# Kernel optimization log

Measured on AMD Instinct MI355X. Metric: run time of the kernel, lower is better.

## Reference

```python
import jax, jax.numpy as jnp
import numpy as np

B, N, D_IN, D_OUT, H = 8, 1024, 768, 768, 12
D_HEAD = D_OUT // H  # 64; per-head softmax scale is sqrt(D_HEAD)


def setup_inputs() -> dict:
    key = jax.random.key(0)
    kx, kq, kk, kv, kwo, kbo = jax.random.split(key, 6)
    s_in = 1.0 / np.sqrt(D_IN)
    s_out = 1.0 / np.sqrt(D_OUT)
    return {
        "x": jax.random.normal(kx, (B, N, D_IN), dtype=jnp.float32),
        # stacked per-head Linear weights, torch layout [out, in] -> [H, d_head, D_IN]
        "Wq": jax.random.uniform(kq, (H, D_HEAD, D_IN), jnp.float32, -s_in, s_in),
        "Wk": jax.random.uniform(kk, (H, D_HEAD, D_IN), jnp.float32, -s_in, s_in),
        "Wv": jax.random.uniform(kv, (H, D_HEAD, D_IN), jnp.float32, -s_in, s_in),
        "Wo": jax.random.uniform(kwo, (D_OUT, D_OUT), jnp.float32, -s_out, s_out),
        "bo": jax.random.uniform(kbo, (D_OUT,), jnp.float32, -s_out, s_out),
    }


def reference(x, Wq, Wk, Wv, Wo, bo):
    # Per-head projections, batched over heads: [B, H, N, d_head]
    q = jnp.einsum('bnd,hed->bhne', x, Wq)
    k = jnp.einsum('bnd,hed->bhne', x, Wk)
    v = jnp.einsum('bnd,hed->bhne', x, Wv)
    scale = 1.0 / np.sqrt(D_HEAD)
    scores = jnp.einsum('bhie,bhje->bhij', q, k) * scale  # [B, H, N, N]
    att = jax.nn.softmax(scores, axis=-1)
    out = jnp.einsum('bhij,bhje->bhie', att, v)  # [B, H, N, d_head]
    # concat heads along last dim: [B, N, H*d_head]
    out = out.transpose(0, 2, 1, 3).reshape(B, N, D_OUT)
    return out @ Wo.T + bo
```

## Files before the change

### kernel.cpp

```cpp
#include <hip/hip_runtime.h>
#include <hip/hip_bf16.h>


typedef unsigned short u16;
typedef unsigned int u32;
typedef __attribute__((ext_vector_type(8))) short bf8;
typedef __attribute__((ext_vector_type(4))) short bf4;
typedef __attribute__((ext_vector_type(4))) float f4;
typedef __attribute__((ext_vector_type(4))) unsigned short us4;

#define NB 8
#define NSEQ 1024
#define DMODEL 768
#define NHEAD 12
#define DHEAD 64

#define XELEMS   (NB * NSEQ * DMODEL)
#define WELEMS   (DMODEL * DMODEL)

__device__ __forceinline__ float b2f(u16 u) {
  union { unsigned int i; float f; } c; c.i = ((unsigned int)u) << 16; return c.f;
}
__device__ __forceinline__ u16 f2b(float f) {
  union { float f; unsigned int i; } c; c.f = f;
  unsigned int r = c.i + 0x7fffu + ((c.i >> 16) & 1u);
  return (u16)(r >> 16);
}
__device__ __forceinline__ void gl_lds16(const u16* g, u16* l) {
  __builtin_amdgcn_global_load_lds(
      (const __attribute__((address_space(1))) unsigned int*)g,
      (__attribute__((address_space(3))) unsigned int*)l, 16, 0, 0);
}

struct CvtArgs {
  const float* src[5];
  u16* dst[5];
};
#define G0 (XELEMS / 4)
#define GW (WELEMS / 4)
#define GTOT (G0 + 4 * GW)

__global__ __launch_bounds__(256) void cvt_kernel(CvtArgs a) {
  size_t g = (size_t)blockIdx.x * 256 + threadIdx.x;
  if (g >= GTOT) return;
  int t; size_t off;
  if (g < G0) { t = 0; off = g; }
  else { size_t r = g - G0; t = 1 + (int)(r / GW); off = r % GW; }
  f4 v = *(const f4*)(a.src[t] + off * 4);
  us4 o;
  o[0] = f2b(v[0]); o[1] = f2b(v[1]); o[2] = f2b(v[2]); o[3] = f2b(v[3]);
  *(us4*)(a.dst[t] + off * 4) = o;
}

__global__ __launch_bounds__(256, 2) void qkv_gemm(
    const u16* __restrict__ x, const u16* __restrict__ Wq,
    const u16* __restrict__ Wk, const u16* __restrict__ Wv,
    u16* __restrict__ q, u16* __restrict__ k, u16* __restrict__ vt)
{
  __shared__ __align__(16) u16 lA[2][128 * 64];
  __shared__ __align__(16) u16 lB[2][128 * 64];

  const int tid  = threadIdx.x;
  const int lane = tid & 63;
  const int w    = tid >> 6;
  const int wm   = w >> 1;
  const int wn   = w & 1;
  const int col  = lane & 15;
  const int quad = lane >> 4;

  const int bid = blockIdx.x;
  const int xcd = bid & 7;
  const int j   = bid >> 3;
  const int bng = j / 48;
  const int rr  = j % 48;
  const int bm8 = rr / 6;
  const int bn6 = rr % 6;
  const int bm  = xcd * 8 + bm8;
  const int bn  = bng * 6 + bn6;

  const int m0 = bm * 128;
  const int proj = bn / 6;
  const u16* Wsel = (proj == 0) ? Wq : (proj == 1 ? Wk : Wv);
  const int nrem0 = (bn % 6) * 128;

  const int srow8 = lane >> 3;
  const int sg    = (lane & 7) ^ srow8;

  const u16* gA = x    + (size_t)(m0    + w * 32 + srow8) * DMODEL + sg * 8;
  const u16* gB = Wsel + (size_t)(nrem0 + w * 32 + srow8) * DMODEL + sg * 8;

  f4 acc[4][4];
#pragma unroll
  for (int i = 0; i < 4; i++)
#pragma unroll
    for (int jj = 0; jj < 4; jj++) acc[i][jj] = (f4)0.0f;

#define QKV_STAGE(T, BUF)                                                      \
  do {                                                                         \
    const int kk_ = (T) * 64;                                                  \
    _Pragma("unroll")                                                          \
    for (int i_ = 0; i_ < 4; i_++)                                             \
      gl_lds16(gA + (size_t)(i_ * 8) * DMODEL + kk_,                           \
               &lA[BUF][(w * 32 + i_ * 8) * 64]);                              \
    _Pragma("unroll")                                                          \
    for (int i_ = 0; i_ < 4; i_++)                                             \
      gl_lds16(gB + (size_t)(i_ * 8) * DMODEL + kk_,                           \
               &lB[BUF][(w * 32 + i_ * 8) * 64]);                              \
  } while (0)

  QKV_STAGE(0, 0);
  __syncthreads();

  for (int t = 0; t < 12; t++) {
    const int cur = t & 1;
    if (t < 11) QKV_STAGE(t + 1, cur ^ 1);

    bf8 af[4][2], bfr[4][2];
#pragma unroll
    for (int mt = 0; mt < 4; mt++) {
      const int row = wm * 64 + mt * 16 + col;
#pragma unroll
      for (int kt = 0; kt < 2; kt++)
        af[mt][kt] = *(const bf8*)&lA[cur][row * 64 + (((kt * 4 + quad) ^ (row & 7)) << 3)];
    }
#pragma unroll
    for (int nt = 0; nt < 4; nt++) {
      const int row = wn * 64 + nt * 16 + col;
#pragma unroll
      for (int kt = 0; kt < 2; kt++)
        bfr[nt][kt] = *(const bf8*)&lB[cur][row * 64 + (((kt * 4 + quad) ^ (row & 7)) << 3)];
    }

    __builtin_amdgcn_s_setprio(1);
#pragma unroll
    for (int mt = 0; mt < 4; mt++)
#pragma unroll
      for (int nt = 0; nt < 4; nt++)
#pragma unroll
        for (int kt = 0; kt < 2; kt++)
          acc[mt][nt] = __builtin_amdgcn_mfma_f32_16x16x32_bf16(af[mt][kt], bfr[nt][kt], acc[mt][nt], 0, 0, 0);
    __builtin_amdgcn_s_setprio(0);

    __syncthreads();
  }
#undef QKV_STAGE

  const int mw0 = m0 + wm * 64, nw0 = nrem0 + wn * 64;
  if (proj == 2) {
#pragma unroll
    for (int mt = 0; mt < 4; mt++) {
#pragma unroll
      for (int nt = 0; nt < 4; nt++) {
        const int nc = nw0 + nt * 16 + col;
        const int h = nc >> 6, e = nc & 63;
        const int t0 = mw0 + mt * 16 + quad * 4;
        const int b = t0 >> 10, tok0 = t0 & 1023;
        us4 pk;
#pragma unroll
        for (int r = 0; r < 4; r++) pk[r] = f2b(acc[mt][nt][r]);
        *(us4*)(vt + ((size_t)(b * NHEAD + h) * DHEAD + e) * NSEQ + tok0) = pk;
      }
    }
  } else {
    u16* dst = (proj == 0) ? q : k;
    const float scl = (proj == 0) ? 0.125f : 1.0f;
#pragma unroll
    for (int mt = 0; mt < 4; mt++) {
#pragma unroll
      for (int nt = 0; nt < 4; nt++) {
        const int nc = nw0 + nt * 16 + col;
        const int h = nc >> 6, e = nc & 63;
#pragma unroll
        for (int r = 0; r < 4; r++) {
          const int t = mw0 + mt * 16 + quad * 4 + r;
          const int b = t >> 10, tok = t & 1023;
          dst[((size_t)(b * NHEAD + h) * NSEQ + tok) * DHEAD + e] = f2b(acc[mt][nt][r] * scl);
        }
      }
    }
  }
}

__global__ __launch_bounds__(256, 3) void attn_kernel(
    const u16* __restrict__ q, const u16* __restrict__ k,
    const u16* __restrict__ vt, u16* __restrict__ attn)
{
  __shared__ __align__(16) u16 ldsK[2][64 * 64];
  __shared__ __align__(16) u16 ldsV[2][64 * 64];
  __shared__ __align__(16) u16 ldsP[4][32][72];

  const int tid  = threadIdx.x;
  const int lane = tid & 63;
  const int w    = tid >> 6;
  const int col  = lane & 15;
  const int quad = lane >> 4;

  const int idx = blockIdx.x;
  const int bh = idx % 96, qc = idx / 96;
  const int b = bh / 12, h = bh % 12;

  const size_t head = ((size_t)b * NHEAD + h) * NSEQ * DHEAD;
  const int q0 = qc * 128 + w * 32;

  const int srow8 = lane >> 3;
  const int sg    = (lane & 7) ^ srow8;

  bf8 onesf;
#pragma unroll
  for (int jj = 0; jj < 8; jj++) onesf[jj] = (short)0x3F80;

  bf8 qf[2][2];
#pragma unroll
  for (int qt = 0; qt < 2; qt++)
#pragma unroll
    for (int kt = 0; kt < 2; kt++) {
      const int row = q0 + qt * 16 + col;
      qf[qt][kt] = *(const bf8*)(q + head + (size_t)row * DHEAD + kt * 32 + quad * 8);
    }

  f4 lacc[2];
  f4 o[2][4];
#pragma unroll
  for (int mt = 0; mt < 2; mt++) {
    lacc[mt] = (f4)0.0f;
#pragma unroll
    for (int et = 0; et < 4; et++) o[mt][et] = (f4)0.0f;
  }

#pragma unroll
  for (int i = 0; i < 2; i++) {
    const int li = w * 2 + i;
    gl_lds16(k  + head + (size_t)(li * 8 + srow8) * DHEAD + sg * 8, &ldsK[0][li * 512]);
    gl_lds16(vt + head + (size_t)(li * 8 + srow8) * NSEQ + sg * 8,  &ldsV[0][li * 512]);
  }

  for (int t = 0; t < NSEQ / 64; t++) {
    const int cur = t & 1;
    __syncthreads();
    if (t < NSEQ / 64 - 1) {
      const int kb2 = (t + 1) * 64;
#pragma unroll
      for (int i = 0; i < 2; i++) {
        const int li = w * 2 + i;
        gl_lds16(k  + head + (size_t)(kb2 + li * 8 + srow8) * DHEAD + sg * 8,
                 &ldsK[cur ^ 1][li * 512]);
        gl_lds16(vt + head + (size_t)(li * 8 + srow8) * NSEQ + kb2 + sg * 8,
                 &ldsV[cur ^ 1][li * 512]);
      }
    }

    f4 st[4][2];
#pragma unroll
    for (int kvt = 0; kvt < 4; kvt++)
#pragma unroll
      for (int qt = 0; qt < 2; qt++) st[kvt][qt] = (f4)0.0f;
#pragma unroll
    for (int kt = 0; kt < 2; kt++) {
      bf8 kf[4];
#pragma unroll
      for (int kvt = 0; kvt < 4; kvt++) {
        const int row = kvt * 16 + col;
        kf[kvt] = *(const bf8*)&ldsK[cur][row * 64 + (((kt * 4 + quad) ^ (col & 7)) << 3)];
      }
      __builtin_amdgcn_s_setprio(1);
#pragma unroll
      for (int kvt = 0; kvt < 4; kvt++)
#pragma unroll
        for (int qt = 0; qt < 2; qt++)
          st[kvt][qt] = __builtin_amdgcn_mfma_f32_16x16x32_bf16(kf[kvt], qf[qt][kt], st[kvt][qt], 0, 0, 0);
      __builtin_amdgcn_s_setprio(0);
    }

#pragma unroll
    for (int kvt = 0; kvt < 4; kvt++)
#pragma unroll
      for (int qt = 0; qt < 2; qt++) {
        const f4 p = st[kvt][qt];
        bf4 pw;
        pw[0] = (short)f2b(__expf(p[0]));
        pw[1] = (short)f2b(__expf(p[1]));
        pw[2] = (short)f2b(__expf(p[2]));
        pw[3] = (short)f2b(__expf(p[3]));
        *(bf4*)&ldsP[w][qt * 16 + col][kvt * 16 + quad * 4] = pw;
      }
    asm volatile("" ::: "memory");

#pragma unroll
    for (int kt2 = 0; kt2 < 2; kt2++) {
      bf8 vf[4];
#pragma unroll
      for (int et = 0; et < 4; et++) {
        const int row = et * 16 + col;
        vf[et] = *(const bf8*)&ldsV[cur][row * 64 + (((kt2 * 4 + quad) ^ (col & 7)) << 3)];
      }
#pragma unroll
      for (int mt = 0; mt < 2; mt++) {
        const bf8 pf = *(const bf8*)&ldsP[w][mt * 16 + col][kt2 * 32 + quad * 8];
        __builtin_amdgcn_s_setprio(1);
        lacc[mt] = __builtin_amdgcn_mfma_f32_16x16x32_bf16(pf, onesf, lacc[mt], 0, 0, 0);
#pragma unroll
        for (int et = 0; et < 4; et++)
          o[mt][et] = __builtin_amdgcn_mfma_f32_16x16x32_bf16(pf, vf[et], o[mt][et], 0, 0, 0);
        __builtin_amdgcn_s_setprio(0);
      }
    }
  }

#pragma unroll
  for (int mt = 0; mt < 2; mt++)
#pragma unroll
    for (int r = 0; r < 4; r++) {
      const float inv = 1.0f / lacc[mt][r];
      const int token = q0 + mt * 16 + quad * 4 + r;
#pragma unroll
      for (int et = 0; et < 4; et++)
        attn[(size_t)(b * NSEQ + token) * DMODEL + h * DHEAD + et * 16 + col] =
            f2b(o[mt][et][r] * inv);
    }
}

__global__ __launch_bounds__(256, 2) void out_gemm(
    const u16* __restrict__ attn, const u16* __restrict__ Wo,
    const float* __restrict__ bo, float* __restrict__ out)
{
  __shared__ __align__(16) u16 lA[2][128 * 64];
  __shared__ __align__(16) u16 lB[2][128 * 64];

  const int tid  = threadIdx.x;
  const int lane = tid & 63;
  const int w    = tid >> 6;
  const int wm   = w >> 1;
  const int wn   = w & 1;
  const int col  = lane & 15;
  const int quad = lane >> 4;

  const int bid = blockIdx.x;
  const int xcd = bid & 7;
  const int j   = bid >> 3;
  const int bm  = xcd * 8 + j / 6;
  const int bn  = j % 6;

  const int m0 = bm * 128;
  const int n0 = bn * 128;

  const int srow8 = lane >> 3;
  const int sg    = (lane & 7) ^ srow8;

  const u16* gA = attn + (size_t)(m0 + w * 32 + srow8) * DMODEL + sg * 8;
  const u16* gB = Wo   + (size_t)(n0 + w * 32 + srow8) * DMODEL + sg * 8;

  f4 acc[4][4];
#pragma unroll
  for (int i = 0; i < 4; i++)
#pragma unroll
    for (int jj = 0; jj < 4; jj++) acc[i][jj] = (f4)0.0f;

#define OUT_STAGE(T, BUF)                                                      \
  do {                                                                         \
    const int kk_ = (T) * 64;                                                  \
    _Pragma("unroll")                                                          \
    for (int i_ = 0; i_ < 4; i_++)                                             \
      gl_lds16(gA + (size_t)(i_ * 8) * DMODEL + kk_,                           \
               &lA[BUF][(w * 32 + i_ * 8) * 64]);                              \
    _Pragma("unroll")                                                          \
    for (int i_ = 0; i_ < 4; i_++)                                             \
      gl_lds16(gB + (size_t)(i_ * 8) * DMODEL + kk_,                           \
               &lB[BUF][(w * 32 + i_ * 8) * 64]);                              \
  } while (0)

  OUT_STAGE(0, 0);
  __syncthreads();

  for (int t = 0; t < 12; t++) {
    const int cur = t & 1;
    if (t < 11) OUT_STAGE(t + 1, cur ^ 1);

    bf8 af[4][2], bfr[4][2];
#pragma unroll
    for (int mt = 0; mt < 4; mt++) {
      const int row = wm * 64 + mt * 16 + col;
#pragma unroll
      for (int kt = 0; kt < 2; kt++)
        af[mt][kt] = *(const bf8*)&lA[cur][row * 64 + (((kt * 4 + quad) ^ (row & 7)) << 3)];
    }
#pragma unroll
    for (int nt = 0; nt < 4; nt++) {
      const int row = wn * 64 + nt * 16 + col;
#pragma unroll
      for (int kt = 0; kt < 2; kt++)
        bfr[nt][kt] = *(const bf8*)&lB[cur][row * 64 + (((kt * 4 + quad) ^ (row & 7)) << 3)];
    }

    __builtin_amdgcn_s_setprio(1);
#pragma unroll
    for (int mt = 0; mt < 4; mt++)
#pragma unroll
      for (int nt = 0; nt < 4; nt++)
#pragma unroll
        for (int kt = 0; kt < 2; kt++)
          acc[mt][nt] = __builtin_amdgcn_mfma_f32_16x16x32_bf16(af[mt][kt], bfr[nt][kt], acc[mt][nt], 0, 0, 0);
    __builtin_amdgcn_s_setprio(0);

    __syncthreads();
  }
#undef OUT_STAGE

  const int mw0 = m0 + wm * 64, nw0 = n0 + wn * 64;
#pragma unroll
  for (int mt = 0; mt < 4; mt++)
#pragma unroll
    for (int nt = 0; nt < 4; nt++) {
      const int n = nw0 + nt * 16 + col;
      const float bias = bo[n];
#pragma unroll
      for (int r = 0; r < 4; r++) {
        const int row = mw0 + mt * 16 + quad * 4 + r;
        out[(size_t)row * DMODEL + n] = acc[mt][nt][r] + bias;
      }
    }
}

extern "C" void kernel_launch(void* const* d_in, const int* in_sizes, int n_in,
                              void* d_out, int out_size, void* d_ws, size_t ws_size,
                              hipStream_t stream) {
  const float* x  = (const float*)d_in[0];
  const float* Wq = (const float*)d_in[1];
  const float* Wk = (const float*)d_in[2];
  const float* Wv = (const float*)d_in[3];
  const float* Wo = (const float*)d_in[4];
  const float* bo = (const float*)d_in[5];
  float* out = (float*)d_out;

  u16* xb   = (u16*)d_ws;
  u16* wqb  = xb  + XELEMS;
  u16* wkb  = wqb + WELEMS;
  u16* wvb  = wkb + WELEMS;
  u16* wob  = wvb + WELEMS;
  u16* q    = wob + WELEMS;
  u16* k    = q   + XELEMS;
  u16* vt   = k   + XELEMS;
  u16* attn = vt  + XELEMS;

  CvtArgs ca;
  ca.src[0] = x;  ca.src[1] = Wq;  ca.src[2] = Wk;  ca.src[3] = Wv;  ca.src[4] = Wo;
  ca.dst[0] = xb; ca.dst[1] = wqb; ca.dst[2] = wkb; ca.dst[3] = wvb; ca.dst[4] = wob;

  cvt_kernel<<<dim3((GTOT + 255) / 256), 256, 0, stream>>>(ca);
  qkv_gemm<<<dim3(1152), 256, 0, stream>>>(xb, wqb, wkb, wvb, q, k, vt);
  attn_kernel<<<dim3(768), 256, 0, stream>>>(q, k, vt, attn);
  out_gemm<<<dim3(384), 256, 0, stream>>>(attn, wob, bo, out);
}
```

Baseline: 189.0 us.

## Shrink attention tiles to 16 queries per wave and 32-key blocks for occupancy

The attention kernel now handles 64 queries per block (16 per wave) and streams K/V in 32-key chunks, with smaller LDS buffers and a re-derived V swizzle. The grid doubles to 1536 blocks and launch bounds rise to 6 blocks per CU, trading per-block reuse for more resident waves to hide latency. Each K/V tile is now reused by fewer queries, so global/LDS traffic per FLOP and sync count per key go up, and the loop runs twice as many iterations with less MFMA work between barriers.

New measurement: 189.5 us. No clear change (+0.3%).

```diff
diff --git a/kernel.cpp b/kernel.cpp
--- a/kernel.cpp
+++ b/kernel.cpp
@@ -181,13 +181,13 @@
   }
 }
 
-__global__ __launch_bounds__(256, 3) void attn_kernel(
+__global__ __launch_bounds__(256, 6) void attn_kernel(
     const u16* __restrict__ q, const u16* __restrict__ k,
     const u16* __restrict__ vt, u16* __restrict__ attn)
 {
-  __shared__ __align__(16) u16 ldsK[2][64 * 64];
-  __shared__ __align__(16) u16 ldsV[2][64 * 64];
-  __shared__ __align__(16) u16 ldsP[4][32][72];
+  __shared__ __align__(16) u16 ldsK[2][32 * 64];
+  __shared__ __align__(16) u16 ldsV[2][64 * 32];
+  __shared__ __align__(16) u16 ldsP[4][16][56];
 
   const int tid  = threadIdx.x;
   const int lane = tid & 63;
@@ -200,123 +200,97 @@
   const int b = bh / 12, h = bh % 12;
 
   const size_t head = ((size_t)b * NHEAD + h) * NSEQ * DHEAD;
-  const int q0 = qc * 128 + w * 32;
+  const int q0 = qc * 64 + w * 16;
 
   const int srow8 = lane >> 3;
-  const int sg    = (lane & 7) ^ srow8;
+  const int sgk   = (lane & 7) ^ srow8;
+  const int srow4 = lane >> 2;
+  const int sgv   = (lane & 3) ^ ((srow4 & 7) >> 1);
+
+  const u16* ksrc = k  + head + (size_t)(w * 8 + srow8) * DHEAD + sgk * 8;
+  const u16* vsrc = vt + head + (size_t)(w * 16 + srow4) * NSEQ + sgv * 8;
 
   bf8 onesf;
 #pragma unroll
   for (int jj = 0; jj < 8; jj++) onesf[jj] = (short)0x3F80;
 
-  bf8 qf[2][2];
-#pragma unroll
-  for (int qt = 0; qt < 2; qt++)
-#pragma unroll
-    for (int kt = 0; kt < 2; kt++) {
-      const int row = q0 + qt * 16 + col;
-      qf[qt][kt] = *(const bf8*)(q + head + (size_t)row * DHEAD + kt * 32 + quad * 8);
-    }
-
-  f4 lacc[2];
-  f4 o[2][4];
-#pragma unroll
-  for (int mt = 0; mt < 2; mt++) {
-    lacc[mt] = (f4)0.0f;
-#pragma unroll
-    for (int et = 0; et < 4; et++) o[mt][et] = (f4)0.0f;
-  }
-
-#pragma unroll
-  for (int i = 0; i < 2; i++) {
-    const int li = w * 2 + i;
-    gl_lds16(k  + head + (size_t)(li * 8 + srow8) * DHEAD + sg * 8, &ldsK[0][li * 512]);
-    gl_lds16(vt + head + (size_t)(li * 8 + srow8) * NSEQ + sg * 8,  &ldsV[0][li * 512]);
-  }
-
-  for (int t = 0; t < NSEQ / 64; t++) {
+  bf8 qf[2];
+#pragma unroll
+  for (int kt = 0; kt < 2; kt++)
+    qf[kt] = *(const bf8*)(q + head + (size_t)(q0 + col) * DHEAD + kt * 32 + quad * 8);
+
+  f4 lacc = (f4)0.0f;
+  f4 o[4];
+#pragma unroll
+  for (int et = 0; et < 4; et++) o[et] = (f4)0.0f;
+
+  gl_lds16(ksrc, &ldsK[0][w * 512]);
+  gl_lds16(vsrc, &ldsV[0][w * 512]);
+
+  for (int t = 0; t < NSEQ / 32; t++) {
     const int cur = t & 1;
     __syncthreads();
-    if (t < NSEQ / 64 - 1) {
-      const int kb2 = (t + 1) * 64;
-#pragma unroll
-      for (int i = 0; i < 2; i++) {
-        const int li = w * 2 + i;
-        gl_lds16(k  + head + (size_t)(kb2 + li * 8 + srow8) * DHEAD + sg * 8,
-                 &ldsK[cur ^ 1][li * 512]);
-        gl_lds16(vt + head + (size_t)(li * 8 + srow8) * NSEQ + kb2 + sg * 8,
-                 &ldsV[cur ^ 1][li * 512]);
-      }
-    }
-
-    f4 st[4][2];
-#pragma unroll
-    for (int kvt = 0; kvt < 4; kvt++)
-#pragma unroll
-      for (int qt = 0; qt < 2; qt++) st[kvt][qt] = (f4)0.0f;
+    if (t < NSEQ / 32 - 1) {
+      const int kv2 = (t + 1) * 32;
+      gl_lds16(ksrc + (size_t)kv2 * DHEAD, &ldsK[cur ^ 1][w * 512]);
+      gl_lds16(vsrc + kv2,                 &ldsV[cur ^ 1][w * 512]);
+    }
+
+    f4 st[2];
+    st[0] = (f4)0.0f; st[1] = (f4)0.0f;
 #pragma unroll
     for (int kt = 0; kt < 2; kt++) {
-      bf8 kf[4];
-#pragma unroll
-      for (int kvt = 0; kvt < 4; kvt++) {
+      bf8 kf[2];
+#pragma unroll
+      for (int kvt = 0; kvt < 2; kvt++) {
         const int row = kvt * 16 + col;
         kf[kvt] = *(const bf8*)&ldsK[cur][row * 64 + (((kt * 4 + quad) ^ (col & 7)) << 3)];
       }
       __builtin_amdgcn_s_setprio(1);
 #pragma unroll
-      for (int kvt = 0; kvt < 4; kvt++)
-#pragma unroll
-        for (int qt = 0; qt < 2; qt++)
-          st[kvt][qt] = __builtin_amdgcn_mfma_f32_16x16x32_bf16(kf[kvt], qf[qt][kt], st[kvt][qt], 0, 0, 0);
+      for (int kvt = 0; kvt < 2; kvt++)
+        st[kvt] = __builtin_amdgcn_mfma_f32_16x16x32_bf16(kf[kvt], qf[kt], st[kvt], 0, 0, 0);
       __builtin_amdgcn_s_setprio(0);
     }
 
 #pragma unroll
-    for (int kvt = 0; kvt < 4; kvt++)
-#pragma unroll
-      for (int qt = 0; qt < 2; qt++) {
-        const f4 p = st[kvt][qt];
-        bf4 pw;
-        pw[0] = (short)f2b(__expf(p[0]));
-        pw[1] = (short)f2b(__expf(p[1]));
-        pw[2] = (short)f2b(__expf(p[2]));
-        pw[3] = (short)f2b(__expf(p[3]));
-        *(bf4*)&ldsP[w][qt * 16 + col][kvt * 16 + quad * 4] = pw;
-      }
+    for (int kvt = 0; kvt < 2; kvt++) {
+      const f4 p = st[kvt];
+      bf4 pw;
+      pw[0] = (short)f2b(__expf(p[0]));
+      pw[1] = (short)f2b(__expf(p[1]));
+      pw[2] = (short)f2b(__expf(p[2]));
+      pw[3] = (short)f2b(__expf(p[3]));
+      *(bf4*)&ldsP[w][col][kvt * 16 + quad * 4] = pw;
+    }
     asm volatile("" ::: "memory");
 
-#pragma unroll
-    for (int kt2 = 0; kt2 < 2; kt2++) {
+    {
+      const bf8 pf = *(const bf8*)&ldsP[w][col][quad * 8];
       bf8 vf[4];
 #pragma unroll
       for (int et = 0; et < 4; et++) {
         const int row = et * 16 + col;
-        vf[et] = *(const bf8*)&ldsV[cur][row * 64 + (((kt2 * 4 + quad) ^ (col & 7)) << 3)];
+        vf[et] = *(const bf8*)&ldsV[cur][row * 32 + ((quad ^ ((col & 7) >> 1)) << 3)];
       }
-#pragma unroll
-      for (int mt = 0; mt < 2; mt++) {
-        const bf8 pf = *(const bf8*)&ldsP[w][mt * 16 + col][kt2 * 32 + quad * 8];
-        __builtin_amdgcn_s_setprio(1);
-        lacc[mt] = __builtin_amdgcn_mfma_f32_16x16x32_bf16(pf, onesf, lacc[mt], 0, 0, 0);
-#pragma unroll
-        for (int et = 0; et < 4; et++)
-          o[mt][et] = __builtin_amdgcn_mfma_f32_16x16x32_bf16(pf, vf[et], o[mt][et], 0, 0, 0);
-        __builtin_amdgcn_s_setprio(0);
-      }
+      __builtin_amdgcn_s_setprio(1);
+      lacc = __builtin_amdgcn_mfma_f32_16x16x32_bf16(pf, onesf, lacc, 0, 0, 0);
+#pragma unroll
+      for (int et = 0; et < 4; et++)
+        o[et] = __builtin_amdgcn_mfma_f32_16x16x32_bf16(pf, vf[et], o[et], 0, 0, 0);
+      __builtin_amdgcn_s_setprio(0);
     }
   }
 
 #pragma unroll
-  for (int mt = 0; mt < 2; mt++)
-#pragma unroll
-    for (int r = 0; r < 4; r++) {
-      const float inv = 1.0f / lacc[mt][r];
-      const int token = q0 + mt * 16 + quad * 4 + r;
-#pragma unroll
-      for (int et = 0; et < 4; et++)
-        attn[(size_t)(b * NSEQ + token) * DMODEL + h * DHEAD + et * 16 + col] =
-            f2b(o[mt][et][r] * inv);
-    }
+  for (int r = 0; r < 4; r++) {
+    const float inv = 1.0f / lacc[r];
+    const int token = q0 + quad * 4 + r;
+#pragma unroll
+    for (int et = 0; et < 4; et++)
+      attn[(size_t)(b * NSEQ + token) * DMODEL + h * DHEAD + et * 16 + col] =
+          f2b(o[et][r] * inv);
+  }
 }
 
 __global__ __launch_bounds__(256, 2) void out_gemm(
@@ -447,6 +421,6 @@
 
   cvt_kernel<<<dim3((GTOT + 255) / 256), 256, 0, stream>>>(ca);
   qkv_gemm<<<dim3(1152), 256, 0, stream>>>(xb, wqb, wkb, wvb, q, k, vt);
-  attn_kernel<<<dim3(768), 256, 0, stream>>>(q, k, vt, attn);
+  attn_kernel<<<dim3(1536), 256, 0, stream>>>(q, k, vt, attn);
   out_gemm<<<dim3(384), 256, 0, stream>>>(attn, wob, bo, out);
 }
```
